# Kernel optimization log

Hardware: AMD Instinct MI355X
Metric: run time of the kernel (lower is better)

Reference implementation:

```python
import jax, jax.numpy as jnp
import numpy as np

B, O, C, HID, H, W = 4, 8, 256, 128, 64, 64
STEPS = 2  # message passing steps


def _conv3x3(x, w, b):
    # x: [N,Cin,H,W], w: [Cout,Cin,3,3]
    y = jax.lax.conv_general_dilated(x, w, window_strides=(1, 1), padding='SAME',
                                     dimension_numbers=('NCHW', 'OIHW', 'NCHW'))
    return y + b[None, :, None, None]


def setup_inputs() -> dict:
    key = jax.random.key(0)
    ks = jax.random.split(key, 6)
    return {
        'batch_node_feats': jax.random.normal(ks[0], (B, C, H, W), jnp.float32),
        'batch_previous_masks': jax.random.uniform(ks[1], (B, O, H, W), jnp.float32),
        'batch_valid_indices': jnp.ones((B, O), jnp.bool_),
        'batch_previous_states': jnp.zeros((B, O), jnp.float32),  # unused (use_temporal_features=False)
        'enc_w': jax.random.normal(ks[2], (HID, C + 1, 3, 3), jnp.float32) * 0.02,
        'enc_b': jnp.zeros((HID,), jnp.float32),
        'gcn_w': jax.random.normal(ks[3], (HID, 2 * HID, 3, 3), jnp.float32) * 0.02,
        'gcn_b': jnp.zeros((HID,), jnp.float32),
        'ro_w': jax.random.normal(ks[4], (1, C + HID, 3, 3), jnp.float32) * 0.02,
        'ro_b': jnp.zeros((1,), jnp.float32),
    }


def reference(batch_node_feats, batch_previous_masks, batch_valid_indices,
              batch_previous_states, enc_w, enc_b, gcn_w, gcn_b, ro_w, ro_b):
    # All objects valid (batch_valid_indices all True) -> fully vectorized over B and O.
    feats = jnp.broadcast_to(batch_node_feats[:, None], (B, O, C, H, W))
    # Mask encoder: per-object state from frame feats + previous object mask.
    enc_in = jnp.concatenate([feats, batch_previous_masks[:, :, None]], axis=2)
    states = jax.nn.relu(_conv3x3(enc_in.reshape(B * O, C + 1, H, W), enc_w, enc_b))
    states = states.reshape(B, O, HID, H, W)
    # Fully-connected message passing: neighbors of i = all objects except i.
    for _ in range(STEPS):
        agg = states.sum(axis=1, keepdims=True) - states  # sum over others
        gcn_in = jnp.concatenate([states, agg], axis=2).reshape(B * O, 2 * HID, H, W)
        states = jax.nn.relu(_conv3x3(gcn_in, gcn_w, gcn_b)).reshape(B, O, HID, H, W)
    # Readout: per-object mask logits -> sigmoid.
    ro_in = jnp.concatenate([feats, states], axis=2).reshape(B * O, C + HID, H, W)
    out_masks = jax.nn.sigmoid(_conv3x3(ro_in, ro_w, ro_b)).reshape(B, O, H, W)
    return out_masks  # out_states is None when use_temporal_features=False
```

## Files before the change

### kernel.cpp

```cpp
#include <hip/hip_runtime.h>
#include <math.h>


typedef unsigned short ushort_t;
typedef _Float16 f16x8 __attribute__((ext_vector_type(8)));
typedef float f32x4 __attribute__((ext_vector_type(4)));

#define GLDS(gsrc, ldst)                                                      \
    __builtin_amdgcn_global_load_lds(                                         \
        (const __attribute__((address_space(1))) unsigned int*)(gsrc),        \
        (__attribute__((address_space(3))) unsigned int*)(ldst), 16, 0, 0)

__device__ __forceinline__ ushort_t f2h(float f) {
    _Float16 h = (_Float16)f;
    return *(ushort_t*)&h;
}
__device__ __forceinline__ float h2f(ushort_t u) {
    _Float16 h = *(_Float16*)&u;
    return (float)h;
}

__global__ __launch_bounds__(256) void prep_weights(
    const float* __restrict__ enc_w, const float* __restrict__ gcn_w,
    const float* __restrict__ ro_w,
    ushort_t* __restrict__ WencF, ushort_t* __restrict__ WgcnS,
    ushort_t* __restrict__ WgcnD, ushort_t* __restrict__ WroQ,
    ushort_t* __restrict__ WroS)
{
    int i = blockIdx.x * 256 + threadIdx.x;
    if (i < 294912) {
        int ci32 = i & 31, co = (i >> 5) & 127, tc = i >> 12;
        int t = tc >> 3, cc = tc & 7, ci = cc * 32 + ci32;
        WencF[i] = f2h(enc_w[(co * 257 + ci) * 9 + t]);
    } else if (i < 442368) {
        int j = i - 294912;
        int ci32 = j & 31, co = (j >> 5) & 127, tc = j >> 12;
        int t = tc >> 2, cc = tc & 3, ci = cc * 32 + ci32;
        WgcnS[j] = f2h(gcn_w[(co * 256 + 128 + ci) * 9 + t]);
    } else if (i < 589824) {
        int j = i - 442368;
        int ci32 = j & 31, co = (j >> 5) & 127, tc = j >> 12;
        int t = tc >> 2, cc = tc & 3, ci = cc * 32 + ci32;
        WgcnD[j] = f2h(gcn_w[(co * 256 + ci) * 9 + t] - gcn_w[(co * 256 + 128 + ci) * 9 + t]);
    } else if (i < 592128) {
        int j = i - 589824;
        int k = j & 7, r = j >> 3;
        int t = r % 9, cq = r / 9, q = cq & 3, cc = cq >> 2;
        WroQ[j] = f2h(ro_w[(cc * 32 + q * 8 + k) * 9 + t]);
    } else if (i < 593280) {
        int j = i - 592128;
        int k = j & 7, r = j >> 3;
        int t = r % 9, cq = r / 9, q = cq & 3, cc = cq >> 2;
        WroS[j] = f2h(ro_w[(256 + cc * 32 + q * 8 + k) * 9 + t]);
    }
}

__global__ __launch_bounds__(256) void feats_to_hwc(const float* __restrict__ feats,
                                                    ushort_t* __restrict__ featsT)
{
    __shared__ float tile[64][65];
    int img = blockIdx.z, ct = blockIdx.y, pt = blockIdx.x;
    int t = threadIdx.x;
    int px_l = t & 63;
    const float* src = feats + ((size_t)img * 256 + ct * 64) * 4096 + pt * 64;
#pragma unroll
    for (int j = 0; j < 16; ++j) {
        int ci_l = (t >> 6) + j * 4;
        tile[px_l][ci_l] = src[(size_t)ci_l * 4096 + px_l];
    }
    __syncthreads();
    int px = t >> 2;
#pragma unroll
    for (int j = 0; j < 2; ++j) {
        int c8 = ((t & 3) + j * 4) * 8;
        uint4 v; ushort_t* pv = (ushort_t*)&v;
#pragma unroll
        for (int k = 0; k < 8; ++k) pv[k] = f2h(tile[px][c8 + k]);
        int cc = ct * 2 + (c8 >> 5);
        *(uint4*)(featsT + ((size_t)img * 8 + cc) * 131072 +
                  (size_t)(pt * 64 + px) * 32 + (c8 & 31)) = v;
    }
}

__global__ __launch_bounds__(256, 3) void conv_mfma(
    const ushort_t* __restrict__ xA, const ushort_t* __restrict__ WA,
    ushort_t* __restrict__ outA, int nA,
    const ushort_t* __restrict__ xB, const ushort_t* __restrict__ WB,
    float* __restrict__ outB, int nB,
    int ncc_img, int ncc_blk)
{
    __shared__ ushort_t raw[25088];
    ushort_t* xs = raw;
    ushort_t* wlds = raw + 16896;
    ushort_t* eb16 = raw;
    float* eb32 = (float*)raw;

    const int rp = blockIdx.x, img = blockIdx.y, kz = blockIdx.z;
    const int row0 = rp * 2;
    const int cc0 = kz * ncc_blk;
    const int nchunk = 9 * ncc_blk;
    const int tid = threadIdx.x;
    const int w = tid >> 6, lane = tid & 63, lq = lane >> 4, lr = lane & 15;
    const int cg = w >> 1, pg = w & 1;

    const bool isA = img < nA;
    const ushort_t* x = isA ? xA + (size_t)img * ncc_img * 131072
                            : xB + (size_t)(img - nA) * ncc_img * 131072;
    const ushort_t* W = isA ? WA : WB;

    const int aoff0 = (cg * 64 + lr) * 32 + lq * 8;

    if (tid < 64) {
        int b = tid >> 5, r = (tid >> 3) & 3, c = (tid >> 2) & 1, s = tid & 3;
        *(uint4*)(xs + b * 8448 + r * 2112 + (c ? 65 : 0) * 32 + s * 8) =
            make_uint4(0, 0, 0, 0);
    }

    f32x4 acc[4][4];
#pragma unroll
    for (int a = 0; a < 4; ++a)
#pragma unroll
        for (int p = 0; p < 4; ++p) acc[a][p] = (f32x4){0.f, 0.f, 0.f, 0.f};

    const int gy = row0 - 1 + w;
    const bool row_ok = (unsigned)gy < 64u;
#define STAGE_ACT(cc_, buf_)                                                    \
    {                                                                           \
        ushort_t* dst = xs + (buf_) * 8448 + w * 2112 + 32;                     \
        if (row_ok) {                                                           \
            const ushort_t* src = x + (size_t)(cc_) * 131072 + (size_t)gy * 2048; \
            GLDS(src + 0 * 512 + lane * 8, dst + 0 * 512);                      \
            GLDS(src + 1 * 512 + lane * 8, dst + 1 * 512);                      \
            GLDS(src + 2 * 512 + lane * 8, dst + 2 * 512);                      \
            GLDS(src + 3 * 512 + lane * 8, dst + 3 * 512);                      \
        } else {                                                                \
            *(uint4*)(dst + 0 * 512 + lane * 8) = make_uint4(0, 0, 0, 0);       \
            *(uint4*)(dst + 1 * 512 + lane * 8) = make_uint4(0, 0, 0, 0);       \
            *(uint4*)(dst + 2 * 512 + lane * 8) = make_uint4(0, 0, 0, 0);       \
            *(uint4*)(dst + 3 * 512 + lane * 8) = make_uint4(0, 0, 0, 0);       \
        }                                                                       \
    }
#define STAGE_W(t_, cc_, buf_)                                                  \
    {                                                                           \
        const ushort_t* src = W + ((size_t)((t_) * ncc_img + (cc_)) * 4096);    \
        ushort_t* dst = wlds + (buf_) * 4096;                                   \
        GLDS(src + (w * 2 + 0) * 512 + lane * 8, dst + (w * 2 + 0) * 512);      \
        GLDS(src + (w * 2 + 1) * 512 + lane * 8, dst + (w * 2 + 1) * 512);      \
    }

    STAGE_ACT(cc0, 0);
    STAGE_W(0, cc0, 0);

    int kc = 0;
    for (int ccl = 0; ccl < ncc_blk; ++ccl) {
        const int cc = cc0 + ccl;
        const int xb = ccl & 1;
#pragma unroll
        for (int t = 0; t < 9; ++t, ++kc) {
            __syncthreads();
            if (kc + 1 < nchunk) {
                if (t == 8) {
                    STAGE_W(0, cc + 1, (kc + 1) & 1);
                    STAGE_ACT(cc + 1, (ccl + 1) & 1);
                } else {
                    STAGE_W(t + 1, cc, (kc + 1) & 1);
                }
            }
            const int dy = t / 3, dx = t - 3 * dy;
            const ushort_t* wl = wlds + (kc & 1) * 4096 + aoff0;
            const ushort_t* xl = xs + xb * 8448 + (pg + dy) * 2112 + (dx + lr) * 32 + lq * 8;
            f16x8 A0 = *(const f16x8*)(wl);
            f16x8 A1 = *(const f16x8*)(wl + 512);
            f16x8 A2 = *(const f16x8*)(wl + 1024);
            f16x8 A3 = *(const f16x8*)(wl + 1536);
#pragma unroll
            for (int p = 0; p < 4; ++p) {
                f16x8 Bf = *(const f16x8*)(xl + p * 512);
                acc[0][p] = __builtin_amdgcn_mfma_f32_16x16x32_f16(A0, Bf, acc[0][p], 0, 0, 0);
                acc[1][p] = __builtin_amdgcn_mfma_f32_16x16x32_f16(A1, Bf, acc[1][p], 0, 0, 0);
                acc[2][p] = __builtin_amdgcn_mfma_f32_16x16x32_f16(A2, Bf, acc[2][p], 0, 0, 0);
                acc[3][p] = __builtin_amdgcn_mfma_f32_16x16x32_f16(A3, Bf, acc[3][p], 0, 0, 0);
            }
        }
    }

    if (isA) {
        ushort_t* obase = outA + (size_t)(kz * nA + img) * 524288;
#pragma unroll
        for (int r = 0; r < 2; ++r) {
            __syncthreads();
            if (pg == r) {
#pragma unroll
                for (int cf = 0; cf < 4; ++cf)
#pragma unroll
                    for (int pf = 0; pf < 4; ++pf) {
                        int px = pf * 16 + lr;
                        int co_l = cg * 64 + cf * 16 + lq * 4;
                        ushort_t pk[4];
#pragma unroll
                        for (int j = 0; j < 4; ++j) pk[j] = f2h(acc[cf][pf][j]);
                        *(uint2*)(eb16 + px * 136 + co_l) = *(uint2*)pk;
                    }
            }
            __syncthreads();
#pragma unroll
            for (int k = 0; k < 4; ++k) {
                int i = tid + k * 256;
                int px = i >> 4, c16 = i & 15;
                uint4 v = *(uint4*)(eb16 + px * 136 + c16 * 8);
                *(uint4*)(obase + (size_t)(c16 >> 2) * 131072 +
                          (size_t)((row0 + r) * 64 + px) * 32 + (c16 & 3) * 8) = v;
            }
        }
    } else {
        float* obase = outB + ((size_t)kz * nB + (img - nA)) * 524288;
#pragma unroll
        for (int r = 0; r < 2; ++r)
#pragma unroll
            for (int h = 0; h < 2; ++h) {
                __syncthreads();
                if (pg == r && cg == h) {
#pragma unroll
                    for (int cf = 0; cf < 4; ++cf)
#pragma unroll
                        for (int pf = 0; pf < 4; ++pf)
                            *(f32x4*)(eb32 + (pf * 16 + lr) * 68 + cf * 16 + lq * 4) =
                                acc[cf][pf];
                }
                __syncthreads();
                for (int i = tid; i < 512; i += 256) {
                    int px = i >> 3, cl = (i & 7) * 8;
                    f32x4 v0 = *(f32x4*)(eb32 + px * 68 + cl);
                    f32x4 v1 = *(f32x4*)(eb32 + px * 68 + cl + 4);
                    float* op = obase + (size_t)((row0 + r) * 64 + px) * 128 + h * 64 + cl;
                    *(f32x4*)op = v0;
                    *(f32x4*)(op + 4) = v1;
                }
            }
    }
#undef STAGE_ACT
#undef STAGE_W
}

__global__ __launch_bounds__(256) void combine_sum(
    ushort_t* __restrict__ S, const float* __restrict__ U2,
    const float* __restrict__ gcn_b, ushort_t* __restrict__ USum)
{
    int i = blockIdx.x * 256 + threadIdx.x;
    int c8 = i & 15, px = (i >> 4) & 4095, b = i >> 16;
    int co = c8 * 8;
    size_t coff = (size_t)(c8 >> 2) * 131072 + (size_t)px * 32 + (c8 & 3) * 8;
    const float* u = U2 + ((size_t)b * 4096 + px) * 128 + co;
    float base[8];
#pragma unroll
    for (int k = 0; k < 8; ++k) base[k] = u[k] + gcn_b[co + k];
    float s[8] = {0, 0, 0, 0, 0, 0, 0, 0};
#pragma unroll
    for (int o = 0; o < 8; ++o) {
        ushort_t* p = S + (size_t)(b * 8 + o) * 524288 + coff;
        uint4 v = *(uint4*)p;
        ushort_t* vp = (ushort_t*)&v;
        uint4 sv; ushort_t* sp = (ushort_t*)&sv;
#pragma unroll
        for (int k = 0; k < 8; ++k) {
            float f = fmaxf(h2f(vp[k]) + base[k], 0.f);
            s[k] += f;
            sp[k] = f2h(f);
        }
        *(uint4*)p = sv;
    }
    uint4 sv; ushort_t* sp = (ushort_t*)&sv;
#pragma unroll
    for (int k = 0; k < 8; ++k) sp[k] = f2h(s[k]);
    *(uint4*)(USum + (size_t)b * 524288 + coff) = sv;
}

__global__ __launch_bounds__(256) void enc_obj_sum(
    const float* __restrict__ masks, const float* __restrict__ enc_w,
    const float* __restrict__ enc_b, const ushort_t* __restrict__ U1p,
    ushort_t* __restrict__ S, ushort_t* __restrict__ USum)
{
    int i = blockIdx.x * 256 + threadIdx.x;
    int c8 = i & 15, px = (i >> 4) & 4095, b = i >> 16;
    int co = c8 * 8;
    int y = px >> 6, xx = px & 63;
    size_t coff = (size_t)(c8 >> 2) * 131072 + (size_t)px * 32 + (c8 & 3) * 8;
    float base[8];
#pragma unroll
    for (int k = 0; k < 8; ++k) base[k] = enc_b[co + k];
#pragma unroll
    for (int p = 0; p < 8; ++p) {
        uint4 v = *(const uint4*)(U1p + (size_t)(p * 4 + b) * 524288 + coff);
        const ushort_t* vp = (const ushort_t*)&v;
#pragma unroll
        for (int k = 0; k < 8; ++k) base[k] += h2f(vp[k]);
    }
    float wm[8][9];
#pragma unroll
    for (int k = 0; k < 8; ++k) {
        const float* wp = enc_w + (size_t)((co + k) * 257 + 256) * 9;
#pragma unroll
        for (int t = 0; t < 9; ++t) wm[k][t] = wp[t];
    }
    float s[8] = {0, 0, 0, 0, 0, 0, 0, 0};
#pragma unroll
    for (int o = 0; o < 8; ++o) {
        const float* m = masks + (size_t)(b * 8 + o) * 4096;
        float mt[9];
#pragma unroll
        for (int dy = 0; dy < 3; ++dy)
#pragma unroll
            for (int dx = 0; dx < 3; ++dx) {
                int gy_ = y + dy - 1, gx = xx + dx - 1;
                mt[dy * 3 + dx] =
                    ((unsigned)gy_ < 64u && (unsigned)gx < 64u) ? m[gy_ * 64 + gx] : 0.f;
            }
        uint4 sv; ushort_t* sp = (ushort_t*)&sv;
#pragma unroll
        for (int k = 0; k < 8; ++k) {
            float acc = base[k];
#pragma unroll
            for (int t = 0; t < 9; ++t) acc = fmaf(mt[t], wm[k][t], acc);
            acc = fmaxf(acc, 0.f);
            s[k] += acc;
            sp[k] = f2h(acc);
        }
        *(uint4*)(S + (size_t)(b * 8 + o) * 524288 + coff) = sv;
    }
    uint4 sv; ushort_t* sp = (ushort_t*)&sv;
#pragma unroll
    for (int k = 0; k < 8; ++k) sp[k] = f2h(s[k]);
    *(uint4*)(USum + (size_t)b * 524288 + coff) = sv;
}

__global__ __launch_bounds__(256) void ro_shared(
    const ushort_t* __restrict__ featsT, const ushort_t* __restrict__ WroQ,
    float* __restrict__ YR)
{
    int i = blockIdx.x * 256 + threadIdx.x;
    int cu = i & 31, px = (i >> 5) & 4095, b = i >> 17;
    int cc = cu >> 2, q = cu & 3;
    int y = px >> 6, xcol = px & 63;
    const ushort_t* wp = WroQ + (size_t)(cc * 4 + q) * 72;
    float wreg[9][8];
#pragma unroll
    for (int t = 0; t < 9; ++t) {
        uint4 wv = *(const uint4*)(wp + t * 8);
        const ushort_t* wq = (const ushort_t*)&wv;
#pragma unroll
        for (int k = 0; k < 8; ++k) wreg[t][k] = h2f(wq[k]);
    }
    const ushort_t* fb = featsT + (size_t)(b * 8 + cc) * 131072 + q * 8;
    float acc = 0.f;
#pragma unroll
    for (int dy = 0; dy < 3; ++dy) {
        int gy = y + dy - 1;
        if ((unsigned)gy >= 64u) continue;
#pragma unroll
        for (int dx = 0; dx < 3; ++dx) {
            int gx = xcol + dx - 1;
            if ((unsigned)gx >= 64u) continue;
            uint4 v = *(const uint4*)(fb + (size_t)(gy * 64 + gx) * 32);
            const ushort_t* vp = (const ushort_t*)&v;
#pragma unroll
            for (int k = 0; k < 8; ++k)
                acc = fmaf(h2f(vp[k]), wreg[dy * 3 + dx][k], acc);
        }
    }
#pragma unroll
    for (int d = 16; d >= 1; d >>= 1) acc += __shfl_down(acc, d, 32);
    if (cu == 0) YR[b * 4096 + px] = acc;
}

__global__ __launch_bounds__(256) void ro_obj(
    const ushort_t* __restrict__ S, const ushort_t* __restrict__ WroS,
    const float* __restrict__ ro_b, const float* __restrict__ YR,
    float* __restrict__ out)
{
    int i = blockIdx.x * 256 + threadIdx.x;
    int cu = i & 15, px = (i >> 4) & 4095, n = i >> 16;
    int b = n >> 3;
    int cc = cu >> 2, q = cu & 3;
    int y = px >> 6, xcol = px & 63;
    const ushort_t* wp = WroS + (size_t)(cc * 4 + q) * 72;
    float wreg[9][8];
#pragma unroll
    for (int t = 0; t < 9; ++t) {
        uint4 wv = *(const uint4*)(wp + t * 8);
        const ushort_t* wq = (const ushort_t*)&wv;
#pragma unroll
        for (int k = 0; k < 8; ++k) wreg[t][k] = h2f(wq[k]);
    }
    const ushort_t* sb = S + ((size_t)n * 4 + cc) * 131072 + q * 8;
    float acc = 0.f;
#pragma unroll
    for (int dy = 0; dy < 3; ++dy) {
        int gy = y + dy - 1;
        if ((unsigned)gy >= 64u) continue;
#pragma unroll
        for (int dx = 0; dx < 3; ++dx) {
            int gx = xcol + dx - 1;
            if ((unsigned)gx >= 64u) continue;
            uint4 v = *(const uint4*)(sb + (size_t)(gy * 64 + gx) * 32);
            const ushort_t* vp = (const ushort_t*)&v;
#pragma unroll
            for (int k = 0; k < 8; ++k)
                acc = fmaf(h2f(vp[k]), wreg[dy * 3 + dx][k], acc);
        }
    }
#pragma unroll
    for (int d = 8; d >= 1; d >>= 1) acc += __shfl_down(acc, d, 16);
    if (cu == 0) {
        float v = acc + YR[b * 4096 + px] + ro_b[0];
        out[n * 4096 + px] = 1.f / (1.f + __expf(-v));
    }
}

extern "C" void kernel_launch(void* const* d_in, const int* in_sizes, int n_in,
                              void* d_out, int out_size, void* d_ws, size_t ws_size,
                              hipStream_t stream)
{
    const float* feats = (const float*)d_in[0];
    const float* masks = (const float*)d_in[1];
    const float* enc_w = (const float*)d_in[4];
    const float* enc_b = (const float*)d_in[5];
    const float* gcn_w = (const float*)d_in[6];
    const float* gcn_b = (const float*)d_in[7];
    const float* ro_w  = (const float*)d_in[8];
    const float* ro_b  = (const float*)d_in[9];
    float* out = (float*)d_out;

    ushort_t* WencF  = (ushort_t*)d_ws;
    ushort_t* WgcnS  = WencF + 294912;
    ushort_t* WgcnD  = WgcnS + 147456;
    ushort_t* WroQ   = WgcnD + 147456;
    ushort_t* WroS   = WroQ + 2304;
    ushort_t* featsT = WroS + 1152;
    ushort_t* Sa     = featsT + 4194304;
    ushort_t* Sb     = Sa + 16777216;
    ushort_t* USum   = Sb + 16777216;
    ushort_t* U1p16  = USum + 2097152;
    float*    U2     = (float*)(U1p16 + 16777216);
    float*    YR     = U2 + 2097152;

    dim3 blk(256);

    prep_weights<<<2320, blk, 0, stream>>>(enc_w, gcn_w, ro_w,
                                           WencF, WgcnS, WgcnD, WroQ, WroS);
    feats_to_hwc<<<dim3(64, 4, 4), blk, 0, stream>>>(feats, featsT);

    conv_mfma<<<dim3(32, 4, 8), blk, 0, stream>>>(
        featsT, WencF, U1p16, 4, nullptr, nullptr, nullptr, 0, 8, 1);
    enc_obj_sum<<<1024, blk, 0, stream>>>(masks, enc_w, enc_b, U1p16, Sa, USum);

    conv_mfma<<<dim3(32, 36, 1), blk, 0, stream>>>(
        Sa, WgcnD, Sb, 32, USum, WgcnS, U2, 4, 4, 4);
    combine_sum<<<1024, blk, 0, stream>>>(Sb, U2, gcn_b, USum);

    conv_mfma<<<dim3(32, 36, 1), blk, 0, stream>>>(
        Sb, WgcnD, Sa, 32, USum, WgcnS, U2, 4, 4, 4);
    combine_sum<<<1024, blk, 0, stream>>>(Sa, U2, gcn_b, USum);

    ro_shared<<<2048, blk, 0, stream>>>(featsT, WroQ, YR);
    ro_obj<<<8192, blk, 0, stream>>>(Sa, WroS, ro_b, YR, out);
}
```

Measured before the change: 272.1 us.

## Split GCN conv into shared-sum and per-object passes, fuse bias/relu epilogue

Merges the weight-prep and feature-transpose kernels into one launch. The shared USum convolution now runs as a separate split-K conv writing fp16 partials. The per-object conv then adds those partials, the bias and relu in its epilogue, which removes the fp32 U2 buffer and the combine_sum read-modify-write pass. A lighter sum8 kernel recomputes the object sum, and it is skipped after the last step. The cost is an extra launch per step plus fp16 rounding of the partial sums, and the per-object conv blocks now do extra global reads in the epilogue.

```diff
diff --git a/kernel.cpp b/kernel.cpp
--- a/kernel.cpp
+++ b/kernel.cpp
@@ -20,94 +20,88 @@
     return (float)h;
 }
 
-__global__ __launch_bounds__(256) void prep_weights(
-    const float* __restrict__ enc_w, const float* __restrict__ gcn_w,
-    const float* __restrict__ ro_w,
-    ushort_t* __restrict__ WencF, ushort_t* __restrict__ WgcnS,
-    ushort_t* __restrict__ WgcnD, ushort_t* __restrict__ WroQ,
-    ushort_t* __restrict__ WroS)
-{
-    int i = blockIdx.x * 256 + threadIdx.x;
+__global__ __launch_bounds__(256) void prep_all(
+    const float* __restrict__ feats, const float* __restrict__ enc_w,
+    const float* __restrict__ gcn_w, const float* __restrict__ ro_w,
+    ushort_t* __restrict__ featsT, ushort_t* __restrict__ WencF,
+    ushort_t* __restrict__ WgcnS, ushort_t* __restrict__ WgcnD,
+    ushort_t* __restrict__ WroQ, ushort_t* __restrict__ WroS)
+{
+    __shared__ float tile[64][65];
+    int bid = blockIdx.x, t = threadIdx.x;
+    if (bid < 1024) {
+        int pt = bid & 63, ct = (bid >> 6) & 3, img = bid >> 8;
+        int px_l = t & 63;
+        const float* src = feats + ((size_t)img * 256 + ct * 64) * 4096 + pt * 64;
+#pragma unroll
+        for (int j = 0; j < 16; ++j) {
+            int ci_l = (t >> 6) + j * 4;
+            tile[px_l][ci_l] = src[(size_t)ci_l * 4096 + px_l];
+        }
+        __syncthreads();
+        int px = t >> 2;
+#pragma unroll
+        for (int j = 0; j < 2; ++j) {
+            int c8 = ((t & 3) + j * 4) * 8;
+            uint4 v; ushort_t* pv = (ushort_t*)&v;
+#pragma unroll
+            for (int k = 0; k < 8; ++k) pv[k] = f2h(tile[px][c8 + k]);
+            int cc = ct * 2 + (c8 >> 5);
+            *(uint4*)(featsT + ((size_t)img * 8 + cc) * 131072 +
+                      (size_t)(pt * 64 + px) * 32 + (c8 & 31)) = v;
+        }
+        return;
+    }
+    int i = (bid - 1024) * 256 + t;
     if (i < 294912) {
         int ci32 = i & 31, co = (i >> 5) & 127, tc = i >> 12;
-        int t = tc >> 3, cc = tc & 7, ci = cc * 32 + ci32;
-        WencF[i] = f2h(enc_w[(co * 257 + ci) * 9 + t]);
+        int tt = tc >> 3, cc = tc & 7, ci = cc * 32 + ci32;
+        WencF[i] = f2h(enc_w[(co * 257 + ci) * 9 + tt]);
     } else if (i < 442368) {
         int j = i - 294912;
         int ci32 = j & 31, co = (j >> 5) & 127, tc = j >> 12;
-        int t = tc >> 2, cc = tc & 3, ci = cc * 32 + ci32;
-        WgcnS[j] = f2h(gcn_w[(co * 256 + 128 + ci) * 9 + t]);
+        int tt = tc >> 2, cc = tc & 3, ci = cc * 32 + ci32;
+        WgcnS[j] = f2h(gcn_w[(co * 256 + 128 + ci) * 9 + tt]);
     } else if (i < 589824) {
         int j = i - 442368;
         int ci32 = j & 31, co = (j >> 5) & 127, tc = j >> 12;
-        int t = tc >> 2, cc = tc & 3, ci = cc * 32 + ci32;
-        WgcnD[j] = f2h(gcn_w[(co * 256 + ci) * 9 + t] - gcn_w[(co * 256 + 128 + ci) * 9 + t]);
+        int tt = tc >> 2, cc = tc & 3, ci = cc * 32 + ci32;
+        WgcnD[j] = f2h(gcn_w[(co * 256 + ci) * 9 + tt] -
+                       gcn_w[(co * 256 + 128 + ci) * 9 + tt]);
     } else if (i < 592128) {
         int j = i - 589824;
         int k = j & 7, r = j >> 3;
-        int t = r % 9, cq = r / 9, q = cq & 3, cc = cq >> 2;
-        WroQ[j] = f2h(ro_w[(cc * 32 + q * 8 + k) * 9 + t]);
+        int tt = r % 9, cq = r / 9, q = cq & 3, cc = cq >> 2;
+        WroQ[j] = f2h(ro_w[(cc * 32 + q * 8 + k) * 9 + tt]);
     } else if (i < 593280) {
         int j = i - 592128;
         int k = j & 7, r = j >> 3;
-        int t = r % 9, cq = r / 9, q = cq & 3, cc = cq >> 2;
-        WroS[j] = f2h(ro_w[(256 + cc * 32 + q * 8 + k) * 9 + t]);
-    }
-}
-
-__global__ __launch_bounds__(256) void feats_to_hwc(const float* __restrict__ feats,
-                                                    ushort_t* __restrict__ featsT)
-{
-    __shared__ float tile[64][65];
-    int img = blockIdx.z, ct = blockIdx.y, pt = blockIdx.x;
-    int t = threadIdx.x;
-    int px_l = t & 63;
-    const float* src = feats + ((size_t)img * 256 + ct * 64) * 4096 + pt * 64;
-#pragma unroll
-    for (int j = 0; j < 16; ++j) {
-        int ci_l = (t >> 6) + j * 4;
-        tile[px_l][ci_l] = src[(size_t)ci_l * 4096 + px_l];
-    }
-    __syncthreads();
-    int px = t >> 2;
-#pragma unroll
-    for (int j = 0; j < 2; ++j) {
-        int c8 = ((t & 3) + j * 4) * 8;
-        uint4 v; ushort_t* pv = (ushort_t*)&v;
-#pragma unroll
-        for (int k = 0; k < 8; ++k) pv[k] = f2h(tile[px][c8 + k]);
-        int cc = ct * 2 + (c8 >> 5);
-        *(uint4*)(featsT + ((size_t)img * 8 + cc) * 131072 +
-                  (size_t)(pt * 64 + px) * 32 + (c8 & 31)) = v;
-    }
-}
-
-__global__ __launch_bounds__(256, 3) void conv_mfma(
-    const ushort_t* __restrict__ xA, const ushort_t* __restrict__ WA,
-    ushort_t* __restrict__ outA, int nA,
-    const ushort_t* __restrict__ xB, const ushort_t* __restrict__ WB,
-    float* __restrict__ outB, int nB,
-    int ncc_img, int ncc_blk)
+        int tt = r % 9, cq = r / 9, q = cq & 3, cc = cq >> 2;
+        WroS[j] = f2h(ro_w[(256 + cc * 32 + q * 8 + k) * 9 + tt]);
+    }
+}
+
+template<int NCCBLK, bool FUSE>
+__global__ __launch_bounds__(256, 3) void conv_k(
+    const ushort_t* __restrict__ x, const ushort_t* __restrict__ W,
+    ushort_t* __restrict__ out,
+    const ushort_t* __restrict__ addp, const float* __restrict__ bias,
+    int ncc_img)
 {
     __shared__ ushort_t raw[25088];
     ushort_t* xs = raw;
     ushort_t* wlds = raw + 16896;
     ushort_t* eb16 = raw;
-    float* eb32 = (float*)raw;
 
     const int rp = blockIdx.x, img = blockIdx.y, kz = blockIdx.z;
     const int row0 = rp * 2;
-    const int cc0 = kz * ncc_blk;
-    const int nchunk = 9 * ncc_blk;
+    const int cc0 = kz * NCCBLK;
+    const int nchunk = 9 * NCCBLK;
     const int tid = threadIdx.x;
     const int w = tid >> 6, lane = tid & 63, lq = lane >> 4, lr = lane & 15;
     const int cg = w >> 1, pg = w & 1;
 
-    const bool isA = img < nA;
-    const ushort_t* x = isA ? xA + (size_t)img * ncc_img * 131072
-                            : xB + (size_t)(img - nA) * ncc_img * 131072;
-    const ushort_t* W = isA ? WA : WB;
-
+    const ushort_t* xb = x + (size_t)img * ncc_img * 131072;
     const int aoff0 = (cg * 64 + lr) * 32 + lq * 8;
 
     if (tid < 64) {
@@ -128,7 +122,7 @@
     {                                                                           \
         ushort_t* dst = xs + (buf_) * 8448 + w * 2112 + 32;                     \
         if (row_ok) {                                                           \
-            const ushort_t* src = x + (size_t)(cc_) * 131072 + (size_t)gy * 2048; \
+            const ushort_t* src = xb + (size_t)(cc_) * 131072 + (size_t)gy * 2048; \
             GLDS(src + 0 * 512 + lane * 8, dst + 0 * 512);                      \
             GLDS(src + 1 * 512 + lane * 8, dst + 1 * 512);                      \
             GLDS(src + 2 * 512 + lane * 8, dst + 2 * 512);                      \
@@ -152,9 +146,10 @@
     STAGE_W(0, cc0, 0);
 
     int kc = 0;
-    for (int ccl = 0; ccl < ncc_blk; ++ccl) {
+#pragma unroll
+    for (int ccl = 0; ccl < NCCBLK; ++ccl) {
         const int cc = cc0 + ccl;
-        const int xb = ccl & 1;
+        const int xbuf = ccl & 1;
 #pragma unroll
         for (int t = 0; t < 9; ++t, ++kc) {
             __syncthreads();
@@ -168,7 +163,7 @@
             }
             const int dy = t / 3, dx = t - 3 * dy;
             const ushort_t* wl = wlds + (kc & 1) * 4096 + aoff0;
-            const ushort_t* xl = xs + xb * 8448 + (pg + dy) * 2112 + (dx + lr) * 32 + lq * 8;
+            const ushort_t* xl = xs + xbuf * 8448 + (pg + dy) * 2112 + (dx + lr) * 32 + lq * 8;
             f16x8 A0 = *(const f16x8*)(wl);
             f16x8 A1 = *(const f16x8*)(wl + 512);
             f16x8 A2 = *(const f16x8*)(wl + 1024);
@@ -184,94 +179,75 @@
         }
     }
 
-    if (isA) {
-        ushort_t* obase = outA + (size_t)(kz * nA + img) * 524288;
-#pragma unroll
-        for (int r = 0; r < 2; ++r) {
-            __syncthreads();
-            if (pg == r) {
-#pragma unroll
-                for (int cf = 0; cf < 4; ++cf)
-#pragma unroll
-                    for (int pf = 0; pf < 4; ++pf) {
-                        int px = pf * 16 + lr;
-                        int co_l = cg * 64 + cf * 16 + lq * 4;
-                        ushort_t pk[4];
-#pragma unroll
-                        for (int j = 0; j < 4; ++j) pk[j] = f2h(acc[cf][pf][j]);
-                        *(uint2*)(eb16 + px * 136 + co_l) = *(uint2*)pk;
-                    }
+    ushort_t* obase = out + (size_t)(kz * gridDim.y + img) * 524288;
+    const int b4 = img >> 3;
+#pragma unroll
+    for (int r = 0; r < 2; ++r) {
+        __syncthreads();
+        if (pg == r) {
+#pragma unroll
+            for (int cf = 0; cf < 4; ++cf)
+#pragma unroll
+                for (int pf = 0; pf < 4; ++pf) {
+                    int px = pf * 16 + lr;
+                    int co_l = cg * 64 + cf * 16 + lq * 4;
+                    ushort_t pk[4];
+#pragma unroll
+                    for (int j = 0; j < 4; ++j) pk[j] = f2h(acc[cf][pf][j]);
+                    *(uint2*)(eb16 + px * 136 + co_l) = *(uint2*)pk;
+                }
+        }
+        __syncthreads();
+#pragma unroll
+        for (int k2 = 0; k2 < 4; ++k2) {
+            int i = tid + k2 * 256;
+            int px = i >> 4, c16 = i & 15;
+            int pxg = (row0 + r) * 64 + px;
+            size_t coff = (size_t)(c16 >> 2) * 131072 + (size_t)pxg * 32 + (c16 & 3) * 8;
+            uint4 v = *(uint4*)(eb16 + px * 136 + c16 * 8);
+            if constexpr (FUSE) {
+                const ushort_t* vp = (const ushort_t*)&v;
+                float vv[8];
+#pragma unroll
+                for (int k = 0; k < 8; ++k) vv[k] = h2f(vp[k]) + bias[c16 * 8 + k];
+#pragma unroll
+                for (int p = 0; p < 4; ++p) {
+                    uint4 av = *(const uint4*)(addp + (size_t)(p * 4 + b4) * 524288 + coff);
+                    const ushort_t* ap = (const ushort_t*)&av;
+#pragma unroll
+                    for (int k = 0; k < 8; ++k) vv[k] += h2f(ap[k]);
+                }
+                uint4 sv; ushort_t* sp = (ushort_t*)&sv;
+#pragma unroll
+                for (int k = 0; k < 8; ++k) sp[k] = f2h(fmaxf(vv[k], 0.f));
+                *(uint4*)(obase + coff) = sv;
+            } else {
+                *(uint4*)(obase + coff) = v;
             }
-            __syncthreads();
-#pragma unroll
-            for (int k = 0; k < 4; ++k) {
-                int i = tid + k * 256;
-                int px = i >> 4, c16 = i & 15;
-                uint4 v = *(uint4*)(eb16 + px * 136 + c16 * 8);
-                *(uint4*)(obase + (size_t)(c16 >> 2) * 131072 +
-                          (size_t)((row0 + r) * 64 + px) * 32 + (c16 & 3) * 8) = v;
-            }
-        }
-    } else {
-        float* obase = outB + ((size_t)kz * nB + (img - nA)) * 524288;
-#pragma unroll
-        for (int r = 0; r < 2; ++r)
-#pragma unroll
-            for (int h = 0; h < 2; ++h) {
-                __syncthreads();
-                if (pg == r && cg == h) {
-#pragma unroll
-                    for (int cf = 0; cf < 4; ++cf)
-#pragma unroll
-                        for (int pf = 0; pf < 4; ++pf)
-                            *(f32x4*)(eb32 + (pf * 16 + lr) * 68 + cf * 16 + lq * 4) =
-                                acc[cf][pf];
-                }
-                __syncthreads();
-                for (int i = tid; i < 512; i += 256) {
-                    int px = i >> 3, cl = (i & 7) * 8;
-                    f32x4 v0 = *(f32x4*)(eb32 + px * 68 + cl);
-                    f32x4 v1 = *(f32x4*)(eb32 + px * 68 + cl + 4);
-                    float* op = obase + (size_t)((row0 + r) * 64 + px) * 128 + h * 64 + cl;
-                    *(f32x4*)op = v0;
-                    *(f32x4*)(op + 4) = v1;
-                }
-            }
+        }
     }
 #undef STAGE_ACT
 #undef STAGE_W
 }
 
-__global__ __launch_bounds__(256) void combine_sum(
-    ushort_t* __restrict__ S, const float* __restrict__ U2,
-    const float* __restrict__ gcn_b, ushort_t* __restrict__ USum)
+__global__ __launch_bounds__(256) void sum8(const ushort_t* __restrict__ S,
+                                            ushort_t* __restrict__ USum)
 {
     int i = blockIdx.x * 256 + threadIdx.x;
-    int c8 = i & 15, px = (i >> 4) & 4095, b = i >> 16;
-    int co = c8 * 8;
-    size_t coff = (size_t)(c8 >> 2) * 131072 + (size_t)px * 32 + (c8 & 3) * 8;
-    const float* u = U2 + ((size_t)b * 4096 + px) * 128 + co;
-    float base[8];
-#pragma unroll
-    for (int k = 0; k < 8; ++k) base[k] = u[k] + gcn_b[co + k];
-    float s[8] = {0, 0, 0, 0, 0, 0, 0, 0};
+    int s = i & 3, px = (i >> 2) & 4095, cc = (i >> 14) & 3, b = i >> 16;
+    size_t coff = (size_t)cc * 131072 + (size_t)px * 32 + s * 8;
+    const ushort_t* p = S + (size_t)b * 8 * 524288 + coff;
+    float v[8] = {0, 0, 0, 0, 0, 0, 0, 0};
 #pragma unroll
     for (int o = 0; o < 8; ++o) {
-        ushort_t* p = S + (size_t)(b * 8 + o) * 524288 + coff;
-        uint4 v = *(uint4*)p;
-        ushort_t* vp = (ushort_t*)&v;
-        uint4 sv; ushort_t* sp = (ushort_t*)&sv;
-#pragma unroll
-        for (int k = 0; k < 8; ++k) {
-            float f = fmaxf(h2f(vp[k]) + base[k], 0.f);
-            s[k] += f;
-            sp[k] = f2h(f);
-        }
-        *(uint4*)p = sv;
+        uint4 xv = *(const uint4*)(p + (size_t)o * 524288);
+        const ushort_t* xp = (const ushort_t*)&xv;
+#pragma unroll
+        for (int k = 0; k < 8; ++k) v[k] += h2f(xp[k]);
     }
     uint4 sv; ushort_t* sp = (ushort_t*)&sv;
 #pragma unroll
-    for (int k = 0; k < 8; ++k) sp[k] = f2h(s[k]);
+    for (int k = 0; k < 8; ++k) sp[k] = f2h(v[k]);
     *(uint4*)(USum + (size_t)b * 524288 + coff) = sv;
 }
 
@@ -281,10 +257,10 @@
     ushort_t* __restrict__ S, ushort_t* __restrict__ USum)
 {
     int i = blockIdx.x * 256 + threadIdx.x;
-    int c8 = i & 15, px = (i >> 4) & 4095, b = i >> 16;
-    int co = c8 * 8;
+    int s = i & 3, px = (i >> 2) & 4095, cc = (i >> 14) & 3, b = i >> 16;
+    int co = cc * 32 + s * 8;
     int y = px >> 6, xx = px & 63;
-    size_t coff = (size_t)(c8 >> 2) * 131072 + (size_t)px * 32 + (c8 & 3) * 8;
+    size_t coff = (size_t)cc * 131072 + (size_t)px * 32 + s * 8;
     float base[8];
 #pragma unroll
     for (int k = 0; k < 8; ++k) base[k] = enc_b[co + k];
@@ -302,7 +278,7 @@
 #pragma unroll
         for (int t = 0; t < 9; ++t) wm[k][t] = wp[t];
     }
-    float s[8] = {0, 0, 0, 0, 0, 0, 0, 0};
+    float sacc[8] = {0, 0, 0, 0, 0, 0, 0, 0};
 #pragma unroll
     for (int o = 0; o < 8; ++o) {
         const float* m = masks + (size_t)(b * 8 + o) * 4096;
@@ -322,14 +298,14 @@
 #pragma unroll
             for (int t = 0; t < 9; ++t) acc = fmaf(mt[t], wm[k][t], acc);
             acc = fmaxf(acc, 0.f);
-            s[k] += acc;
+            sacc[k] += acc;
             sp[k] = f2h(acc);
         }
         *(uint4*)(S + (size_t)(b * 8 + o) * 524288 + coff) = sv;
     }
     uint4 sv; ushort_t* sp = (ushort_t*)&sv;
 #pragma unroll
-    for (int k = 0; k < 8; ++k) sp[k] = f2h(s[k]);
+    for (int k = 0; k < 8; ++k) sp[k] = f2h(sacc[k]);
     *(uint4*)(USum + (size_t)b * 524288 + coff) = sv;
 }
 
@@ -440,26 +416,28 @@
     ushort_t* Sb     = Sa + 16777216;
     ushort_t* USum   = Sb + 16777216;
     ushort_t* U1p16  = USum + 2097152;
-    float*    U2     = (float*)(U1p16 + 16777216);
-    float*    YR     = U2 + 2097152;
+    ushort_t* U2p16  = U1p16 + 16777216;
+    float*    YR     = (float*)(U2p16 + 8388608);
 
     dim3 blk(256);
 
-    prep_weights<<<2320, blk, 0, stream>>>(enc_w, gcn_w, ro_w,
-                                           WencF, WgcnS, WgcnD, WroQ, WroS);
-    feats_to_hwc<<<dim3(64, 4, 4), blk, 0, stream>>>(feats, featsT);
-
-    conv_mfma<<<dim3(32, 4, 8), blk, 0, stream>>>(
-        featsT, WencF, U1p16, 4, nullptr, nullptr, nullptr, 0, 8, 1);
+    prep_all<<<3344, blk, 0, stream>>>(feats, enc_w, gcn_w, ro_w,
+                                       featsT, WencF, WgcnS, WgcnD, WroQ, WroS);
+
+    conv_k<1, false><<<dim3(32, 4, 8), blk, 0, stream>>>(
+        featsT, WencF, U1p16, nullptr, nullptr, 8);
     enc_obj_sum<<<1024, blk, 0, stream>>>(masks, enc_w, enc_b, U1p16, Sa, USum);
 
-    conv_mfma<<<dim3(32, 36, 1), blk, 0, stream>>>(
-        Sa, WgcnD, Sb, 32, USum, WgcnS, U2, 4, 4, 4);
-    combine_sum<<<1024, blk, 0, stream>>>(Sb, U2, gcn_b, USum);
-
-    conv_mfma<<<dim3(32, 36, 1), blk, 0, stream>>>(
-        Sb, WgcnD, Sa, 32, USum, WgcnS, U2, 4, 4, 4);
-    combine_sum<<<1024, blk, 0, stream>>>(Sa, U2, gcn_b, USum);
+    conv_k<1, false><<<dim3(32, 4, 4), blk, 0, stream>>>(
+        USum, WgcnS, U2p16, nullptr, nullptr, 4);
+    conv_k<4, true><<<dim3(32, 32, 1), blk, 0, stream>>>(
+        Sa, WgcnD, Sb, U2p16, gcn_b, 4);
+    sum8<<<1024, blk, 0, stream>>>(Sb, USum);
+
+    conv_k<1, false><<<dim3(32, 4, 4), blk, 0, stream>>>(
+        USum, WgcnS, U2p16, nullptr, nullptr, 4);
+    conv_k<4, true><<<dim3(32, 32, 1), blk, 0, stream>>>(
+        Sb, WgcnD, Sa, U2p16, gcn_b, 4);
 
     ro_shared<<<2048, blk, 0, stream>>>(featsT, WroQ, YR);
     ro_obj<<<8192, blk, 0, stream>>>(Sa, WroS, ro_b, YR, out);
```

After: 272.9 us. About the same (+0.3%).
